# Kernel optimization log

Measured on AMD Instinct MI355X. Metric: run time of the kernel, lower is better.

## Reference

```python
import jax, jax.numpy as jnp
import numpy as np

NUM_HEADS = 16
HEAD_DIM = 64
LN_EPS = 1e-5


def setup_inputs() -> dict:
    key = jax.random.key(0)
    k1, k2, k3, k4 = jax.random.split(key, 4)
    B, N, D = 4, 2048, NUM_HEADS * HEAD_DIM
    q = jax.random.normal(k1, (B, N, D), dtype=jnp.float32)
    k = jax.random.normal(k2, (B, N, D), dtype=jnp.float32)
    v = jax.random.normal(k3, (B, N, D), dtype=jnp.float32)
    W_out = jax.random.normal(k4, (D, D), dtype=jnp.float32) * (1.0 / np.sqrt(D))
    g = jnp.ones((D,), dtype=jnp.float32)
    return {"q": q, "k": k, "v": v, "W_out": W_out, "g": g}


def _split_heads(x):
    b, n, _ = x.shape
    return x.reshape(b, n, NUM_HEADS, HEAD_DIM).transpose(0, 2, 1, 3)  # b h n d


def reference(q, k, v, W_out, g):
    scale = HEAD_DIM ** -0.5
    qh = _split_heads(q) * scale          # [b,h,n,d]
    kh = _split_heads(k)                  # [b,h,m,d]
    vh = _split_heads(v)                  # [b,h,m,d]
    sim = jnp.einsum('bhnd,bhmd->bhnm', qh, kh)
    attn = jax.nn.softmax(sim.astype(jnp.float32), axis=-1)
    out = jnp.einsum('bhnm,bhmd->bhnd', attn, vh)
    b, h, n, d = out.shape
    out = out.transpose(0, 2, 1, 3).reshape(b, n, h * d)  # b n (h d)
    out = out @ W_out.T                   # Linear, no bias
    # LayerNorm (bias=False), biased variance
    mean = jnp.mean(out, axis=-1, keepdims=True)
    var = jnp.var(out, axis=-1, keepdims=True)
    return (out - mean) * jax.lax.rsqrt(var + LN_EPS) * g
```

## Files before the change

### kernel.cpp

```cpp
#include <hip/hip_runtime.h>
#include <hip/hip_bf16.h>


#define Bv 4
#define Nv 2048
#define Hv 16
#define DHv 64
#define Dv 1024
#define NT (Nv / 64)

#define KCONV_BLOCKS 4096
#define WCONV_BLOCKS 512
#define VT_BLOCKS 2048

typedef __attribute__((ext_vector_type(8))) short short8;
typedef __attribute__((ext_vector_type(4))) float floatx4;

__device__ inline unsigned pack_bf2(float a, float b) {
    unsigned ua = __builtin_bit_cast(unsigned, a) + 0x8000u;
    unsigned ub = __builtin_bit_cast(unsigned, b) + 0x8000u;
    return __builtin_amdgcn_perm(ub, ua, 0x07060302u);
}

__device__ inline void plswap16(unsigned &a, unsigned &b) {
    auto r = __builtin_amdgcn_permlane16_swap(a, b, false, false);
    a = r[0]; b = r[1];
}
__device__ inline void plswap32(unsigned &a, unsigned &b) {
    auto r = __builtin_amdgcn_permlane32_swap(a, b, false, false);
    a = r[0]; b = r[1];
}

__device__ inline float redq_max(float x) {
    unsigned a = __builtin_bit_cast(unsigned, x), b = a;
    plswap16(a, b);
    float m = fmaxf(__builtin_bit_cast(float, a), __builtin_bit_cast(float, b));
    unsigned c = __builtin_bit_cast(unsigned, m), d = c;
    plswap32(c, d);
    return fmaxf(__builtin_bit_cast(float, c), __builtin_bit_cast(float, d));
}
__device__ inline float redq_sum(float x) {
    unsigned a = __builtin_bit_cast(unsigned, x), b = a;
    plswap16(a, b);
    float m = __builtin_bit_cast(float, a) + __builtin_bit_cast(float, b);
    unsigned c = __builtin_bit_cast(unsigned, m), d = c;
    plswap32(c, d);
    return __builtin_bit_cast(float, c) + __builtin_bit_cast(float, d);
}

__global__ __launch_bounds__(256)
void prep_all(const float* __restrict__ K, __hip_bfloat16* __restrict__ Kb,
              const float* __restrict__ W, __hip_bfloat16* __restrict__ Wb,
              const float* __restrict__ v, __hip_bfloat16* __restrict__ vt) {
    __shared__ short T[64][72];
    int bid = blockIdx.x;
    if (bid < KCONV_BLOCKS + WCONV_BLOCKS) {
        const float* src;
        __hip_bfloat16* dst;
        if (bid < KCONV_BLOCKS) { src = K; dst = Kb; }
        else { src = W; dst = Wb; bid -= KCONV_BLOCKS; }
        int base = (bid * 256 + threadIdx.x) * 8;
        float4 f0 = *(const float4*)(src + base);
        float4 f1 = *(const float4*)(src + base + 4);
        uint4 u;
        u.x = pack_bf2(f0.x, f0.y);
        u.y = pack_bf2(f0.z, f0.w);
        u.z = pack_bf2(f1.x, f1.y);
        u.w = pack_bf2(f1.z, f1.w);
        *(uint4*)(dst + base) = u;
        return;
    }
    bid -= KCONV_BLOCKS + WCONV_BLOCKS;
    const int b = bid >> 9;
    const int rem = bid & 511;
    const int h = rem >> 5;
    const int n0 = (rem & 31) * 64;
    const int t = threadIdx.x;
    const int ir = t >> 4;
    const int d4 = (t & 15) * 4;
#pragma unroll
    for (int pass = 0; pass < 4; ++pass) {
        int n = pass * 16 + ir;
        float4 f = *(const float4*)(v + ((size_t)b * Nv + n0 + n) * Dv + h * DHv + d4);
        T[d4 + 0][n] = (short)(pack_bf2(f.x, f.x) & 0xffffu);
        T[d4 + 1][n] = (short)(pack_bf2(f.y, f.y) & 0xffffu);
        T[d4 + 2][n] = (short)(pack_bf2(f.z, f.z) & 0xffffu);
        T[d4 + 3][n] = (short)(pack_bf2(f.w, f.w) & 0xffffu);
    }
    __syncthreads();
    const int d = t >> 2, kg = (t & 3) * 16;
    unsigned u[8];
#pragma unroll
    for (int i = 0; i < 8; ++i)
        u[i] = (unsigned)(unsigned short)T[d][kg + 2 * i] |
               ((unsigned)(unsigned short)T[d][kg + 2 * i + 1] << 16);
    __hip_bfloat16* op = vt + ((size_t)(b * Hv + h) * DHv + d) * Nv + n0 + kg;
    *(uint4*)op = *(uint4*)&u[0];
    *(uint4*)(op + 8) = *(uint4*)&u[4];
}

__global__ __launch_bounds__(256)
void attn_mfma_pre(const float* __restrict__ q,
                   const __hip_bfloat16* __restrict__ Kb,
                   const __hip_bfloat16* __restrict__ Vtb,
                   __hip_bfloat16* __restrict__ out) {
    __shared__ __align__(16) short Kt[2][64 * 64];
    __shared__ __align__(16) short Vt[2][64 * 64];

    const int t = threadIdx.x;
    const int wave = t >> 6, lane = t & 63;
    const int quad = lane >> 4, lr = lane & 15;
    const int b = blockIdx.z;
    const int lid2 = blockIdx.y * 16 + blockIdx.x;
    const int xcd = lid2 & 7, jj = lid2 >> 3;
    const int h = xcd * 2 + (jj >> 4);
    const int q0 = (jj & 15) * 128;
    const size_t qbh = ((size_t)b * Nv) * Dv + h * DHv;
    const __hip_bfloat16* kb = Kb + (size_t)b * Nv * Dv + h * DHv;
    const __hip_bfloat16* vtb = Vtb + (size_t)(b * Hv + h) * DHv * Nv;

    const int srow = lane >> 3;
    const int sg = lane & 7;
    auto stage = [&](int buf, int k0) {
#pragma unroll
        for (int c = 0; c < 2; ++c) {
            int blk = wave * 2 + c;
            int r = blk * 8 + srow;
            int g = sg ^ (r & 7);
            __builtin_amdgcn_global_load_lds(
                (const __attribute__((address_space(1))) unsigned*)(const void*)
                    (kb + (size_t)(k0 + r) * Dv + g * 8),
                (__attribute__((address_space(3))) unsigned*)(void*)&Kt[buf][blk * 512],
                16, 0, 0);
            __builtin_amdgcn_global_load_lds(
                (const __attribute__((address_space(1))) unsigned*)(const void*)
                    (vtb + (size_t)r * Nv + k0 + g * 8),
                (__attribute__((address_space(3))) unsigned*)(void*)&Vt[buf][blk * 512],
                16, 0, 0);
        }
    };

    stage(0, 0);

    short8 qfrag[2][2];
#pragma unroll
    for (int qs = 0; qs < 2; ++qs)
#pragma unroll
        for (int kh = 0; kh < 2; ++kh) {
            int row = q0 + wave * 32 + qs * 16 + lr;
            const float* qp = q + qbh + (size_t)row * Dv + kh * 32 + quad * 8;
            float4 f0 = *(const float4*)qp;
            float4 f1 = *(const float4*)(qp + 4);
            int4 qi;
            qi.x = (int)pack_bf2(f0.x * 0.125f, f0.y * 0.125f);
            qi.y = (int)pack_bf2(f0.z * 0.125f, f0.w * 0.125f);
            qi.z = (int)pack_bf2(f1.x * 0.125f, f1.y * 0.125f);
            qi.w = (int)pack_bf2(f1.z * 0.125f, f1.w * 0.125f);
            qfrag[qs][kh] = __builtin_bit_cast(short8, qi);
        }

    floatx4 o_acc[2][4] = {};
    float mrow[2] = {-INFINITY, -INFINITY};
    float lrow[2] = {0.f, 0.f};

    for (int it = 0; it < NT; ++it) {
        const int cur = it & 1;
        __syncthreads();
        if (it + 1 < NT) stage(1 - cur, (it + 1) * 64);

        floatx4 s_acc[2][4] = {};
#pragma unroll
        for (int tt = 0; tt < 4; ++tt) {
            int row = tt * 16 + lr;
            short8 kf0 = *(const short8*)&Kt[cur][row * 64 + ((quad ^ (lr & 7)) << 3)];
            short8 kf1 = *(const short8*)&Kt[cur][row * 64 + (((4 + quad) ^ (lr & 7)) << 3)];
#pragma unroll
            for (int qs = 0; qs < 2; ++qs) {
                s_acc[qs][tt] = __builtin_amdgcn_mfma_f32_16x16x32_bf16(kf0, qfrag[qs][0], s_acc[qs][tt], 0, 0, 0);
                s_acc[qs][tt] = __builtin_amdgcn_mfma_f32_16x16x32_bf16(kf1, qfrag[qs][1], s_acc[qs][tt], 0, 0, 0);
            }
        }

        unsigned p2[2][8];
#pragma unroll
        for (int qs = 0; qs < 2; ++qs) {
            float t4[4];
#pragma unroll
            for (int tt = 0; tt < 4; ++tt)
                t4[tt] = fmaxf(fmaxf(s_acc[qs][tt][0], s_acc[qs][tt][1]),
                               fmaxf(s_acc[qs][tt][2], s_acc[qs][tt][3]));
            float tmax = fmaxf(fmaxf(t4[0], t4[1]), fmaxf(t4[2], t4[3]));
            tmax = redq_max(tmax);
            float mnew = fmaxf(mrow[qs], tmax);
            float alpha = __expf(mrow[qs] - mnew);
            mrow[qs] = mnew;
            float psum = 0.f;
#pragma unroll
            for (int tt = 0; tt < 4; ++tt)
#pragma unroll
                for (int r2 = 0; r2 < 4; ++r2) {
                    float p = __expf(s_acc[qs][tt][r2] - mnew);
                    s_acc[qs][tt][r2] = p;
                    psum += p;
                }
            psum = redq_sum(psum);
            lrow[qs] = lrow[qs] * alpha + psum;
#pragma unroll
            for (int r2 = 0; r2 < 4; ++r2) {
                float ar = __shfl(alpha, quad * 4 + r2);
#pragma unroll
                for (int td = 0; td < 4; ++td) o_acc[qs][td][r2] *= ar;
            }
#pragma unroll
            for (int tt = 0; tt < 4; ++tt) {
                p2[qs][tt * 2 + 0] = pack_bf2(s_acc[qs][tt][0], s_acc[qs][tt][1]);
                p2[qs][tt * 2 + 1] = pack_bf2(s_acc[qs][tt][2], s_acc[qs][tt][3]);
            }
        }

#pragma unroll
        for (int kh = 0; kh < 2; ++kh) {
            short8 af[2];
#pragma unroll
            for (int qs = 0; qs < 2; ++qs) {
                int tlo = 4 * kh, thi = 4 * kh + 2;
                unsigned a0 = p2[qs][tlo + 0], b0 = p2[qs][thi + 0];
                unsigned a1 = p2[qs][tlo + 1], b1 = p2[qs][thi + 1];
                plswap32(a0, b0);
                plswap16(a0, b0);
                plswap32(a1, b1);
                plswap16(a1, b1);
                int4 afi;
                afi.x = (int)a0;
                afi.y = (int)a1;
                afi.z = (int)b0;
                afi.w = (int)b1;
                af[qs] = __builtin_bit_cast(short8, afi);
            }
#pragma unroll
            for (int td = 0; td < 4; ++td) {
                int d = td * 16 + lr;
                short8 vf = *(const short8*)&Vt[cur][d * 64 + (((kh * 4 + quad) ^ (lr & 7)) << 3)];
                o_acc[0][td] = __builtin_amdgcn_mfma_f32_16x16x32_bf16(af[0], vf, o_acc[0][td], 0, 0, 0);
                o_acc[1][td] = __builtin_amdgcn_mfma_f32_16x16x32_bf16(af[1], vf, o_acc[1][td], 0, 0, 0);
            }
        }
    }

#pragma unroll
    for (int qs = 0; qs < 2; ++qs) {
        float linv = 1.f / lrow[qs];
#pragma unroll
        for (int r2 = 0; r2 < 4; ++r2) {
            float lv = __shfl(linv, quad * 4 + r2);
            int row = q0 + wave * 32 + qs * 16 + quad * 4 + r2;
            size_t base = ((size_t)(b * Nv + row)) * Dv + h * DHv;
#pragma unroll
            for (int td = 0; td < 4; ++td)
                out[base + td * 16 + lr] = __float2bfloat16(o_acc[qs][td][r2] * lv);
        }
    }
}

__global__ __launch_bounds__(256)
void proj_kernel(const __hip_bfloat16* __restrict__ A,
                 const __hip_bfloat16* __restrict__ Wb,
                 float* __restrict__ C) {
    __shared__ __align__(16) short As[2][128 * 64];
    __shared__ __align__(16) short Ws[2][128 * 64];

    const int t = threadIdx.x;
    const int wave = t >> 6, lane = t & 63;
    const int quad = lane >> 4, lr = lane & 15;
    const int wm = wave >> 1, wn = wave & 1;
    const int bm = blockIdx.y * 128;
    const int bn = blockIdx.x * 128;

    floatx4 acc[4][4] = {};

    auto stage = [&](int buf, int k0) {
#pragma unroll
        for (int c = 0; c < 4; ++c) {
            const int blk = c * 4 + wave;
            const int r = blk * 8 + (lane >> 3);
            const int g = (lane & 7) ^ (r & 7);
            const __hip_bfloat16* ga = A + (size_t)(bm + r) * Dv + k0 + g * 8;
            const __hip_bfloat16* gw = Wb + (size_t)(bn + r) * Dv + k0 + g * 8;
            __builtin_amdgcn_global_load_lds(
                (const __attribute__((address_space(1))) unsigned int*)(const void*)ga,
                (__attribute__((address_space(3))) unsigned int*)(void*)&As[buf][blk * 512],
                16, 0, 0);
            __builtin_amdgcn_global_load_lds(
                (const __attribute__((address_space(1))) unsigned int*)(const void*)gw,
                (__attribute__((address_space(3))) unsigned int*)(void*)&Ws[buf][blk * 512],
                16, 0, 0);
        }
    };

    stage(0, 0);

    for (int it = 0; it < Dv / 64; ++it) {
        const int cur = it & 1;
        __syncthreads();
        if (it + 1 < Dv / 64) stage(1 - cur, (it + 1) * 64);

#pragma unroll
        for (int ks = 0; ks < 2; ++ks) {
            short8 af[4];
#pragma unroll
            for (int mb = 0; mb < 4; ++mb) {
                int row = wm * 64 + mb * 16 + lr;
                af[mb] = *(const short8*)&As[cur][row * 64 + (((ks * 4 + quad) ^ (lr & 7)) << 3)];
            }
#pragma unroll
            for (int nb = 0; nb < 4; ++nb) {
                int row = wn * 64 + nb * 16 + lr;
                short8 bf = *(const short8*)&Ws[cur][row * 64 + (((ks * 4 + quad) ^ (lr & 7)) << 3)];
#pragma unroll
                for (int mb = 0; mb < 4; ++mb)
                    acc[mb][nb] = __builtin_amdgcn_mfma_f32_16x16x32_bf16(af[mb], bf, acc[mb][nb], 0, 0, 0);
            }
        }
    }

#pragma unroll
    for (int mb = 0; mb < 4; ++mb)
#pragma unroll
        for (int nb = 0; nb < 4; ++nb) {
            int row = bm + wm * 64 + mb * 16 + quad * 4;
            int col = bn + wn * 64 + nb * 16 + lr;
#pragma unroll
            for (int r = 0; r < 4; ++r)
                C[(size_t)(row + r) * Dv + col] = acc[mb][nb][r];
        }
}

__global__ __launch_bounds__(256)
void ln_kernel(float* __restrict__ C,
               const float* __restrict__ g) {
    const int row = blockIdx.x;
    const int t = threadIdx.x;
    const int wave = t >> 6, lane = t & 63;

    float* rp = C + (size_t)row * Dv;
    float4 x = *(const float4*)(rp + t * 4);

    float s = x.x + x.y + x.z + x.w;
    float sq = x.x * x.x + x.y * x.y + x.z * x.z + x.w * x.w;
#pragma unroll
    for (int off = 32; off >= 1; off >>= 1) {
        s += __shfl_xor(s, off);
        sq += __shfl_xor(sq, off);
    }
    __shared__ float ss[4], ssq[4];
    if (lane == 0) { ss[wave] = s; ssq[wave] = sq; }
    __syncthreads();
    s = ss[0] + ss[1] + ss[2] + ss[3];
    sq = ssq[0] + ssq[1] + ssq[2] + ssq[3];

    const float rn = 1.f / (float)Dv;
    float mean = s * rn;
    float var = sq * rn - mean * mean;
    float inv = rsqrtf(var + 1e-5f);

    float4 gv = *(const float4*)(g + t * 4);

    float4 o;
    o.x = (x.x - mean) * inv * gv.x;
    o.y = (x.y - mean) * inv * gv.y;
    o.z = (x.z - mean) * inv * gv.z;
    o.w = (x.w - mean) * inv * gv.w;
    *(float4*)(rp + t * 4) = o;
}

extern "C" void kernel_launch(void* const* d_in, const int* in_sizes, int n_in,
                              void* d_out, int out_size, void* d_ws, size_t ws_size,
                              hipStream_t stream) {
    const float* q = (const float*)d_in[0];
    const float* k = (const float*)d_in[1];
    const float* v = (const float*)d_in[2];
    const float* W = (const float*)d_in[3];
    const float* g = (const float*)d_in[4];
    float* out = (float*)d_out;

    const size_t attnB = (size_t)Bv * Nv * Dv * 2;
    const size_t wbB = (size_t)Dv * Dv * 2;
    const size_t kbB = (size_t)Bv * Nv * Dv * 2;

    __hip_bfloat16* attn = (__hip_bfloat16*)d_ws;
    __hip_bfloat16* Wb = (__hip_bfloat16*)((char*)d_ws + attnB);
    __hip_bfloat16* Kb = (__hip_bfloat16*)((char*)d_ws + attnB + wbB);
    __hip_bfloat16* Vtb = (__hip_bfloat16*)((char*)d_ws + attnB + wbB + kbB);

    prep_all<<<KCONV_BLOCKS + WCONV_BLOCKS + VT_BLOCKS, 256, 0, stream>>>(k, Kb, W, Wb, v, Vtb);
    attn_mfma_pre<<<dim3(16, 16, Bv), 256, 0, stream>>>(q, Kb, Vtb, attn);
    proj_kernel<<<dim3(Dv / 128, (Bv * Nv) / 128), 256, 0, stream>>>(attn, Wb, out);
    ln_kernel<<<Bv * Nv, 256, 0, stream>>>(out, g);
}
```

Measured before the change: 317.7 us.

## Lazy softmax rescale, exp2 softmax, transposed PV MFMA, XCD-aware proj block mapping

The online softmax now rescales the output accumulator and running sum only when some lane's new max exceeds the stored max by more than 8, and computes exponentials with exp2 and a pre-scaled max. The PV MFMA operands are swapped so each lane holds one query row, which removes the per-row shuffles for alpha and 1/l and lets the output be written as packed 8-byte stores. The projection GEMM uses a 1D grid remapped so that neighbouring M tiles land on the same XCD for better L2 reuse. The trade-off is that exponentials can reach up to e^8 while rescaling is deferred, which loosens numerical headroom, plus a wave-uniform branch in the inner loop.

```diff
diff --git a/kernel.cpp b/kernel.cpp
--- a/kernel.cpp
+++ b/kernel.cpp
@@ -13,6 +13,8 @@
 #define WCONV_BLOCKS 512
 #define VT_BLOCKS 2048
 
+#define L2E 1.44269504088896340736f
+
 typedef __attribute__((ext_vector_type(8))) short short8;
 typedef __attribute__((ext_vector_type(4))) float floatx4;
 
@@ -20,6 +22,12 @@
     unsigned ua = __builtin_bit_cast(unsigned, a) + 0x8000u;
     unsigned ub = __builtin_bit_cast(unsigned, b) + 0x8000u;
     return __builtin_amdgcn_perm(ub, ua, 0x07060302u);
+}
+
+__device__ inline unsigned bf2u_rte(float a, float b) {
+    unsigned short ua = __builtin_bit_cast(unsigned short, __float2bfloat16(a));
+    unsigned short ub = __builtin_bit_cast(unsigned short, __float2bfloat16(b));
+    return (unsigned)ua | ((unsigned)ub << 16);
 }
 
 __device__ inline void plswap16(unsigned &a, unsigned &b) {
@@ -191,26 +199,28 @@
                                fmaxf(s_acc[qs][tt][2], s_acc[qs][tt][3]));
             float tmax = fmaxf(fmaxf(t4[0], t4[1]), fmaxf(t4[2], t4[3]));
             tmax = redq_max(tmax);
-            float mnew = fmaxf(mrow[qs], tmax);
-            float alpha = __expf(mrow[qs] - mnew);
-            mrow[qs] = mnew;
+            if (!__all(tmax <= mrow[qs] + 8.0f)) {
+                float mnew = fmaxf(mrow[qs], tmax);
+                float alpha = __expf(mrow[qs] - mnew);
+                mrow[qs] = mnew;
+                lrow[qs] *= alpha;
+#pragma unroll
+                for (int td = 0; td < 4; ++td)
+#pragma unroll
+                    for (int r2 = 0; r2 < 4; ++r2) o_acc[qs][td][r2] *= alpha;
+            }
+            float mc = mrow[qs] * L2E;
             float psum = 0.f;
 #pragma unroll
             for (int tt = 0; tt < 4; ++tt)
 #pragma unroll
                 for (int r2 = 0; r2 < 4; ++r2) {
-                    float p = __expf(s_acc[qs][tt][r2] - mnew);
+                    float p = __builtin_amdgcn_exp2f(__builtin_fmaf(s_acc[qs][tt][r2], L2E, -mc));
                     s_acc[qs][tt][r2] = p;
                     psum += p;
                 }
             psum = redq_sum(psum);
-            lrow[qs] = lrow[qs] * alpha + psum;
-#pragma unroll
-            for (int r2 = 0; r2 < 4; ++r2) {
-                float ar = __shfl(alpha, quad * 4 + r2);
-#pragma unroll
-                for (int td = 0; td < 4; ++td) o_acc[qs][td][r2] *= ar;
-            }
+            lrow[qs] += psum;
 #pragma unroll
             for (int tt = 0; tt < 4; ++tt) {
                 p2[qs][tt * 2 + 0] = pack_bf2(s_acc[qs][tt][0], s_acc[qs][tt][1]);
@@ -241,8 +251,8 @@
             for (int td = 0; td < 4; ++td) {
                 int d = td * 16 + lr;
                 short8 vf = *(const short8*)&Vt[cur][d * 64 + (((kh * 4 + quad) ^ (lr & 7)) << 3)];
-                o_acc[0][td] = __builtin_amdgcn_mfma_f32_16x16x32_bf16(af[0], vf, o_acc[0][td], 0, 0, 0);
-                o_acc[1][td] = __builtin_amdgcn_mfma_f32_16x16x32_bf16(af[1], vf, o_acc[1][td], 0, 0, 0);
+                o_acc[0][td] = __builtin_amdgcn_mfma_f32_16x16x32_bf16(vf, af[0], o_acc[0][td], 0, 0, 0);
+                o_acc[1][td] = __builtin_amdgcn_mfma_f32_16x16x32_bf16(vf, af[1], o_acc[1][td], 0, 0, 0);
             }
         }
     }
@@ -250,14 +260,14 @@
 #pragma unroll
     for (int qs = 0; qs < 2; ++qs) {
         float linv = 1.f / lrow[qs];
-#pragma unroll
-        for (int r2 = 0; r2 < 4; ++r2) {
-            float lv = __shfl(linv, quad * 4 + r2);
-            int row = q0 + wave * 32 + qs * 16 + quad * 4 + r2;
-            size_t base = ((size_t)(b * Nv + row)) * Dv + h * DHv;
-#pragma unroll
-            for (int td = 0; td < 4; ++td)
-                out[base + td * 16 + lr] = __float2bfloat16(o_acc[qs][td][r2] * lv);
+        int qrow = q0 + wave * 32 + qs * 16 + lr;
+        __hip_bfloat16* op = out + ((size_t)(b * Nv + qrow)) * Dv + h * DHv + quad * 4;
+#pragma unroll
+        for (int td = 0; td < 4; ++td) {
+            uint2 w;
+            w.x = bf2u_rte(o_acc[qs][td][0] * linv, o_acc[qs][td][1] * linv);
+            w.y = bf2u_rte(o_acc[qs][td][2] * linv, o_acc[qs][td][3] * linv);
+            *(uint2*)(op + td * 16) = w;
         }
     }
 }
@@ -273,8 +283,10 @@
     const int wave = t >> 6, lane = t & 63;
     const int quad = lane >> 4, lr = lane & 15;
     const int wm = wave >> 1, wn = wave & 1;
-    const int bm = blockIdx.y * 128;
-    const int bn = blockIdx.x * 128;
+    const int bx = blockIdx.x;
+    const int xcd = bx & 7, j = bx >> 3;
+    const int bm = (xcd * 8 + (j >> 3)) * 128;
+    const int bn = (j & 7) * 128;
 
     floatx4 acc[4][4] = {};
 
@@ -394,6 +406,6 @@
 
     prep_all<<<KCONV_BLOCKS + WCONV_BLOCKS + VT_BLOCKS, 256, 0, stream>>>(k, Kb, W, Wb, v, Vtb);
     attn_mfma_pre<<<dim3(16, 16, Bv), 256, 0, stream>>>(q, Kb, Vtb, attn);
-    proj_kernel<<<dim3(Dv / 128, (Bv * Nv) / 128), 256, 0, stream>>>(attn, Wb, out);
+    proj_kernel<<<512, 256, 0, stream>>>(attn, Wb, out);
     ln_kernel<<<Bv * Nv, 256, 0, stream>>>(out, g);
 }
```

Measured after the change: 295.1 us. -7.1%, faster.
